# Optimization experiments

Hardware: AMD Instinct MI355X
Metric: run time of the kernel (lower is better)

Reference implementation:

```python
import jax, jax.numpy as jnp
import numpy as np

NUM_EMBEDDINGS = 1024
EMBEDDING_DIM = 256
COMMITMENT_COST = 0.25


def setup_inputs() -> dict:
    key = jax.random.key(0)
    k_z, k_e = jax.random.split(key)
    z = jax.random.normal(k_z, (8, EMBEDDING_DIM, 16, 16, 16), dtype=jnp.float32)
    # nn.Embedding weight initialized uniform(-1/K, 1/K)
    codebook = jax.random.uniform(
        k_e, (NUM_EMBEDDINGS, EMBEDDING_DIM), dtype=jnp.float32,
        minval=-1.0 / NUM_EMBEDDINGS, maxval=1.0 / NUM_EMBEDDINGS)
    return {"z": z, "codebook": codebook}


def reference(z, codebook):
    B, D, H, W, L = z.shape
    # (B, D, H, W, L) -> (B, H, W, L, D) -> (N, D)
    z_perm = jnp.transpose(z, (0, 2, 3, 4, 1))          # (B,H,W,L,D)
    z_flat = z_perm.reshape(-1, D)                       # (N,D)
    # squared-distance via expansion: ||z||^2 + ||e||^2 - 2 z.e^T
    distances = ((z_flat ** 2).sum(axis=1, keepdims=True)
                 + (codebook ** 2).sum(axis=1)
                 - 2.0 * z_flat @ codebook.T)            # (N,K)
    indices = jnp.argmin(distances, axis=1)              # (N,)
    quantized = codebook[indices].reshape(B, H, W, L, D)
    idx_out = indices.reshape(B, H, W, L)
    # losses (stop_gradient mirrors .detach())
    e_latent_loss = jnp.mean((jax.lax.stop_gradient(quantized) - z_perm) ** 2)
    q_latent_loss = jnp.mean((quantized - jax.lax.stop_gradient(z_perm)) ** 2)
    vq_loss = q_latent_loss + COMMITMENT_COST * e_latent_loss
    # straight-through estimator
    quant_st = z_perm + jax.lax.stop_gradient(quantized - z_perm)
    quant_out = jnp.transpose(quant_st, (0, 4, 1, 2, 3))  # (B,D,H,W,L)
    return quant_out, idx_out, vq_loss
```

## Files before the change

### kernel.cpp

```cpp
#include <hip/hip_runtime.h>
#include <hip/hip_bf16.h>


#define K_CODES 1024
#define DIM 256
#define N_TOK 32768
#define SPATIAL 4096
#define TOK_BLK 64
#define CAP 28
#define MARGIN 1e-3f

typedef __attribute__((ext_vector_type(8))) short short8;
typedef __attribute__((ext_vector_type(4))) float float4v;

#define WS_LOSS 0
#define WS_E2 16
#define WS_EB 2048

#define O_IDX (8 * DIM * SPATIAL)
#define O_LOSS (O_IDX + N_TOK)

__device__ __forceinline__ float np_pairwise128(const float* x) {
  float r[8];
#pragma unroll
  for (int j = 0; j < 8; j++) r[j] = x[j];
  for (int i = 8; i < 128; i += 8) {
#pragma unroll
    for (int j = 0; j < 8; j++) r[j] = __fadd_rn(r[j], x[i + j]);
  }
  return __fadd_rn(__fadd_rn(__fadd_rn(r[0], r[1]), __fadd_rn(r[2], r[3])),
                   __fadd_rn(__fadd_rn(r[4], r[5]), __fadd_rn(r[6], r[7])));
}

__device__ __forceinline__ short f2bf(float v) {
  unsigned u = __float_as_uint(v);
  u = (u + 0x7fffu + ((u >> 16) & 1u)) >> 16;
  return (short)u;
}

__global__ __launch_bounds__(256) void prep_kernel(const float* __restrict__ e,
                                                   float* __restrict__ ws) {
  __shared__ float sq[DIM];
  int k = blockIdx.x, d = threadIdx.x;
  float v = e[k * DIM + d];
  int stage = k >> 6, ct = (k >> 4) & 3, nn = k & 15;
  int f = d >> 5, q = (d >> 3) & 3, j = d & 7;
  int off = ((((stage * 4 + ct) * 8 + f) * 64 + (q * 16 + nn)) * 8 + j);
  ((short*)(ws + WS_EB))[off] = f2bf(v);
  sq[d] = __fmul_rn(v, v);
  __syncthreads();
  if (d == 0) {
    ws[WS_E2 + k] = __fadd_rn(np_pairwise128(sq), np_pairwise128(sq + 128));
    if (k == 0) ws[WS_LOSS] = 0.f;
  }
}

__global__ __launch_bounds__(256, 2) void main_kernel(const float* __restrict__ z,
                                                      const float* __restrict__ e,
                                                      float* __restrict__ ws,
                                                      float* __restrict__ out) {
  __shared__ __align__(16) short Bst[64 * 256];
  __shared__ unsigned short cand[TOK_BLK][CAP];
  __shared__ float cands[TOK_BLK][CAP];
  __shared__ float aminv[TOK_BLK];
  __shared__ int cnt[TOK_BLK];
  __shared__ float Szs[TOK_BLK];
  __shared__ int mini_sh[TOK_BLK];
  __shared__ float red[4];

  int tid = threadIdx.x, w = tid >> 6, lane = tid & 63;
  int quad = lane >> 4, nn = lane & 15;
  int n0 = blockIdx.x * TOK_BLK;
  int b = n0 >> 12, s0 = n0 & 4095;
  const float* zb = z + (size_t)b * DIM * SPATIAL + s0;
  const float* Se = ws + WS_E2;
  if (tid < TOK_BLK) cnt[tid] = 0;

  if (quad == 0) {
    const float* zp = zb + w * 16 + nn;
    float total = 0.f;
#pragma unroll
    for (int blk = 0; blk < 2; blk++) {
      float r[8];
#pragma unroll
      for (int j = 0; j < 8; j++) {
        float v = zp[(size_t)(blk * 128 + j) * SPATIAL];
        r[j] = __fmul_rn(v, v);
      }
      for (int i = 8; i < 128; i += 8) {
#pragma unroll
        for (int j = 0; j < 8; j++) {
          float v = zp[(size_t)(blk * 128 + i + j) * SPATIAL];
          r[j] = __fadd_rn(r[j], __fmul_rn(v, v));
        }
      }
      float res = __fadd_rn(__fadd_rn(__fadd_rn(r[0], r[1]), __fadd_rn(r[2], r[3])),
                            __fadd_rn(__fadd_rn(r[4], r[5]), __fadd_rn(r[6], r[7])));
      total = (blk == 0) ? res : __fadd_rn(total, res);
    }
    Szs[w * 16 + nn] = total;
  }

  int tokA = w * 16 + nn;
  short8 A[8];
#pragma unroll
  for (int f = 0; f < 8; f++) {
    short8 a;
#pragma unroll
    for (int j = 0; j < 8; j++) {
      int d = f * 32 + quad * 8 + j;
      a[j] = f2bf(zb[(size_t)d * SPATIAL + tokA]);
    }
    A[f] = a;
  }

  const uint4* eBg = (const uint4*)(ws + WS_EB);
  float thr[4] = {3.4e38f, 3.4e38f, 3.4e38f, 3.4e38f};
  for (int stage = 0; stage < 16; stage++) {
    __syncthreads();
#pragma unroll
    for (int i = 0; i < 8; i++)
      ((uint4*)Bst)[i * 256 + tid] = eBg[(size_t)stage * 2048 + i * 256 + tid];
    __syncthreads();

    for (int ct = 0; ct < 4; ct++) {
      int kbase = stage * 64 + ct * 16;
      float4v C = {0.f, 0.f, 0.f, 0.f};
      const short8* Bp = (const short8*)Bst + ct * 8 * 64;
#pragma unroll
      for (int f = 0; f < 8; f++) {
        short8 Bf = Bp[f * 64 + lane];
        C = __builtin_amdgcn_mfma_f32_16x16x32_bf16(A[f], Bf, C, 0, 0, 0);
      }
      float SeK = Se[kbase + nn];
      float sv[4];
      bool pr[4];
#pragma unroll
      for (int r = 0; r < 4; r++) {
        float s = fmaf(-2.f, C[r], SeK);
        float m = s;
        m = fminf(m, __shfl_xor(m, 1, 16));
        m = fminf(m, __shfl_xor(m, 2, 16));
        m = fminf(m, __shfl_xor(m, 4, 16));
        m = fminf(m, __shfl_xor(m, 8, 16));
        thr[r] = fminf(thr[r], m);
        sv[r] = s;
        pr[r] = s < thr[r] + MARGIN;
      }
      if (__ballot(pr[0] | pr[1] | pr[2] | pr[3])) {
#pragma unroll
        for (int r = 0; r < 4; r++) {
          unsigned long long bl = __ballot(pr[r]);
          unsigned grp = (unsigned)((bl >> (quad * 16)) & 0xffffULL);
          if (grp) {
            int tb = w * 16 + quad * 4 + r;
            int base = cnt[tb];
            if (pr[r]) {
              int pos = base + __popc(grp & ((1u << nn) - 1u));
              if (pos < CAP) {
                cand[tb][pos] = (unsigned short)(kbase + nn);
                cands[tb][pos] = sv[r];
              }
            }
            if (nn == 0) cnt[tb] = base + __popc(grp);
          }
        }
      }
    }
  }
#pragma unroll
  for (int r = 0; r < 4; r++)
    if (nn == 0) aminv[w * 16 + quad * 4 + r] = thr[r];

  int tb = w * 16 + nn;
  int cc = cnt[tb];
  int cl = cc < CAP ? cc : CAP;
  float bestD = 3.4e38f;
  int bestk = 0x7fffffff;
  {
    const float* zp = zb + tb;
    float amin = aminv[tb], Szn = Szs[tb];
    for (int c = quad; c < cl; c += 4) {
      if (cands[tb][c] >= amin + MARGIN) continue;
      int k = cand[tb][c];
      const float* er = e + (size_t)k * DIM;
      float acc = 0.f;
      for (int d = 0; d < DIM; d++) acc = fmaf(zp[(size_t)d * SPATIAL], er[d], acc);
      float D = __fsub_rn(__fadd_rn(Szn, Se[k]), __fmul_rn(2.f, acc));
      if (D < bestD || (D == bestD && k < bestk)) { bestD = D; bestk = k; }
    }
  }
#pragma unroll
  for (int off = 32; off >= 16; off >>= 1) {
    float oD = __shfl_down(bestD, off);
    int ok = __shfl_down(bestk, off);
    if (oD < bestD || (oD == bestD && ok < bestk)) { bestD = oD; bestk = ok; }
  }
  if (lane < 16 && cnt[w * 16 + lane] <= CAP) {
    mini_sh[w * 16 + lane] = bestk;
    out[O_IDX + n0 + w * 16 + lane] = (float)bestk;
  }
  for (int t = 0; t < 16; t++) {
    int tb2 = w * 16 + t;
    if (cnt[tb2] > CAP) {
      const float* zq = zb + tb2;
      float Szn = Szs[tb2];
      float bD = 3.4e38f;
      int bk = 0x7fffffff;
      for (int k = lane; k < K_CODES; k += 64) {
        const float* er = e + (size_t)k * DIM;
        float acc = 0.f;
        for (int d = 0; d < DIM; d++) acc = fmaf(zq[(size_t)d * SPATIAL], er[d], acc);
        float D = __fsub_rn(__fadd_rn(Szn, Se[k]), __fmul_rn(2.f, acc));
        if (D < bD || (D == bD && k < bk)) { bD = D; bk = k; }
      }
#pragma unroll
      for (int m = 1; m < 64; m <<= 1) {
        float oD = __shfl_xor(bD, m);
        int ok = __shfl_xor(bk, m);
        if (oD < bD || (oD == bD && ok < bk)) { bD = oD; bk = ok; }
      }
      if (lane == 0) {
        mini_sh[tb2] = bk;
        out[O_IDX + n0 + tb2] = (float)bk;
      }
    }
  }
  __syncthreads();

  int mten = mini_sh[lane];
  const float* erow = e + (size_t)mten * DIM;
  float* op = out + (size_t)b * DIM * SPATIAL + s0;
  float sumsq = 0.f;
  for (int i = 0; i < 64; i++) {
    int d = w * 64 + i;
    float v = erow[d];
    float zv = zb[(size_t)d * SPATIAL + lane];
    float df = __fsub_rn(v, zv);
    sumsq = fmaf(df, df, sumsq);
    op[(size_t)d * SPATIAL + lane] = v;
  }
#pragma unroll
  for (int o = 32; o > 0; o >>= 1) sumsq += __shfl_down(sumsq, o, 64);
  if (lane == 0) red[w] = sumsq;
  __syncthreads();
  if (tid == 0) atomicAdd(ws + WS_LOSS, red[0] + red[1] + red[2] + red[3]);
}

__global__ void loss_kernel(const float* __restrict__ ws, float* __restrict__ out) {
  out[O_LOSS] = 1.25f * ws[WS_LOSS] / 8388608.f;
}

extern "C" void kernel_launch(void* const* d_in, const int* in_sizes, int n_in,
                              void* d_out, int out_size, void* d_ws, size_t ws_size,
                              hipStream_t stream) {
  const float* z = (const float*)d_in[0];
  const float* e = (const float*)d_in[1];
  float* ws = (float*)d_ws;
  float* out = (float*)d_out;

  prep_kernel<<<K_CODES, 256, 0, stream>>>(e, ws);
  main_kernel<<<N_TOK / TOK_BLK, 256, 0, stream>>>(z, e, ws, out);
  loss_kernel<<<1, 1, 0, stream>>>(ws, out);
}
```

Baseline: 206.7 us.

## Double-buffer codebook stages via async LDS loads, parallelize norms, fuse loss kernel

Codebook bf16 tiles are now loaded straight into LDS with global_load_lds into two buffers, and the next-but-one stage is issued after each compute stage, so loads overlap the MFMA work. The z-norm computation is spread across all four quads with shuffle reduction instead of one quad, and prep writes 16-byte chunks. The separate loss kernel is removed; the last block, found with an atomic counter, writes the final loss. Unroll pragmas are added to the exact-rescore loops. The LDS footprint doubles, which may limit occupancy, and the hand-written waitcnt logic adds risk.

```diff
diff --git a/kernel.cpp b/kernel.cpp
--- a/kernel.cpp
+++ b/kernel.cpp
@@ -1,5 +1,4 @@
 #include <hip/hip_runtime.h>
-#include <hip/hip_bf16.h>
 
 
 #define K_CODES 1024
@@ -7,6 +6,7 @@
 #define N_TOK 32768
 #define SPATIAL 4096
 #define TOK_BLK 64
+#define NBLK (N_TOK / TOK_BLK)
 #define CAP 28
 #define MARGIN 1e-3f
 
@@ -14,23 +14,12 @@
 typedef __attribute__((ext_vector_type(4))) float float4v;
 
 #define WS_LOSS 0
+#define WS_CNT 8
 #define WS_E2 16
 #define WS_EB 2048
 
 #define O_IDX (8 * DIM * SPATIAL)
 #define O_LOSS (O_IDX + N_TOK)
-
-__device__ __forceinline__ float np_pairwise128(const float* x) {
-  float r[8];
-#pragma unroll
-  for (int j = 0; j < 8; j++) r[j] = x[j];
-  for (int i = 8; i < 128; i += 8) {
-#pragma unroll
-    for (int j = 0; j < 8; j++) r[j] = __fadd_rn(r[j], x[i + j]);
-  }
-  return __fadd_rn(__fadd_rn(__fadd_rn(r[0], r[1]), __fadd_rn(r[2], r[3])),
-                   __fadd_rn(__fadd_rn(r[4], r[5]), __fadd_rn(r[6], r[7])));
-}
 
 __device__ __forceinline__ short f2bf(float v) {
   unsigned u = __float_as_uint(v);
@@ -38,20 +27,58 @@
   return (short)u;
 }
 
+__device__ __forceinline__ void gload_lds16(const void* g, void* l) {
+  __builtin_amdgcn_global_load_lds(
+      (__attribute__((address_space(1))) unsigned*)g,
+      (__attribute__((address_space(3))) unsigned*)l, 16, 0, 0);
+}
+
+__device__ __forceinline__ void stage_issue(const uint4* eBg, short* lbuf,
+                                            int stage, int tid) {
+#pragma unroll
+  for (int i = 0; i < 8; i++)
+    gload_lds16(eBg + (size_t)stage * 2048 + i * 256 + tid,
+                lbuf + ((i * 256 + tid) << 3));
+}
+
 __global__ __launch_bounds__(256) void prep_kernel(const float* __restrict__ e,
                                                    float* __restrict__ ws) {
   __shared__ float sq[DIM];
+  __shared__ __align__(16) short sbf[DIM];
+  __shared__ float chv[16];
   int k = blockIdx.x, d = threadIdx.x;
   float v = e[k * DIM + d];
-  int stage = k >> 6, ct = (k >> 4) & 3, nn = k & 15;
-  int f = d >> 5, q = (d >> 3) & 3, j = d & 7;
-  int off = ((((stage * 4 + ct) * 8 + f) * 64 + (q * 16 + nn)) * 8 + j);
-  ((short*)(ws + WS_EB))[off] = f2bf(v);
+  sbf[d] = f2bf(v);
   sq[d] = __fmul_rn(v, v);
   __syncthreads();
+  if (d < 32) {
+    int f = d >> 2, q = d & 3;
+    int stage = k >> 6, ct = (k >> 4) & 3, nn = k & 15;
+    short8 chunk = *(const short8*)(sbf + f * 32 + q * 8);
+    int off8 = ((stage * 4 + ct) * 8 + f) * 64 + q * 16 + nn;
+    ((short8*)(ws + WS_EB))[off8] = chunk;
+  }
+  if (d < 16) {
+    int blkb = d >> 3, j = d & 7;
+    const float* x = sq + blkb * 128;
+    float c = x[j];
+#pragma unroll
+    for (int i = 1; i < 16; i++) c = __fadd_rn(c, x[i * 8 + j]);
+    chv[d] = c;
+  }
+  __syncthreads();
   if (d == 0) {
-    ws[WS_E2 + k] = __fadd_rn(np_pairwise128(sq), np_pairwise128(sq + 128));
-    if (k == 0) ws[WS_LOSS] = 0.f;
+    float a0 = __fadd_rn(__fadd_rn(chv[0], chv[1]), __fadd_rn(chv[2], chv[3]));
+    float a1 = __fadd_rn(__fadd_rn(chv[4], chv[5]), __fadd_rn(chv[6], chv[7]));
+    float resA = __fadd_rn(a0, a1);
+    float b0 = __fadd_rn(__fadd_rn(chv[8], chv[9]), __fadd_rn(chv[10], chv[11]));
+    float b1 = __fadd_rn(__fadd_rn(chv[12], chv[13]), __fadd_rn(chv[14], chv[15]));
+    float resB = __fadd_rn(b0, b1);
+    ws[WS_E2 + k] = __fadd_rn(resA, resB);
+    if (k == 0) {
+      ws[WS_LOSS] = 0.f;
+      ((unsigned*)ws)[WS_CNT] = 0u;
+    }
   }
 }
 
@@ -59,7 +86,7 @@
                                                       const float* __restrict__ e,
                                                       float* __restrict__ ws,
                                                       float* __restrict__ out) {
-  __shared__ __align__(16) short Bst[64 * 256];
+  __shared__ __align__(16) short Bst[2][64 * 256];
   __shared__ unsigned short cand[TOK_BLK][CAP];
   __shared__ float cands[TOK_BLK][CAP];
   __shared__ float aminv[TOK_BLK];
@@ -74,31 +101,32 @@
   int b = n0 >> 12, s0 = n0 & 4095;
   const float* zb = z + (size_t)b * DIM * SPATIAL + s0;
   const float* Se = ws + WS_E2;
+  const uint4* eBg = (const uint4*)(ws + WS_EB);
   if (tid < TOK_BLK) cnt[tid] = 0;
 
-  if (quad == 0) {
+  stage_issue(eBg, Bst[0], 0, tid);
+  stage_issue(eBg, Bst[1], 1, tid);
+  __builtin_amdgcn_sched_barrier(0);
+
+  {
     const float* zp = zb + w * 16 + nn;
-    float total = 0.f;
-#pragma unroll
-    for (int blk = 0; blk < 2; blk++) {
-      float r[8];
-#pragma unroll
-      for (int j = 0; j < 8; j++) {
-        float v = zp[(size_t)(blk * 128 + j) * SPATIAL];
-        r[j] = __fmul_rn(v, v);
-      }
-      for (int i = 8; i < 128; i += 8) {
-#pragma unroll
-        for (int j = 0; j < 8; j++) {
-          float v = zp[(size_t)(blk * 128 + i + j) * SPATIAL];
-          r[j] = __fadd_rn(r[j], __fmul_rn(v, v));
-        }
-      }
-      float res = __fadd_rn(__fadd_rn(__fadd_rn(r[0], r[1]), __fadd_rn(r[2], r[3])),
-                            __fadd_rn(__fadd_rn(r[4], r[5]), __fadd_rn(r[6], r[7])));
-      total = (blk == 0) ? res : __fadd_rn(total, res);
-    }
-    Szs[w * 16 + nn] = total;
+    float r[4];
+#pragma unroll
+    for (int t = 0; t < 4; t++) {
+      int c = quad * 4 + t, blkb = c >> 3, j = c & 7;
+      float v0 = zp[(size_t)(blkb * 128 + j) * SPATIAL];
+      r[t] = __fmul_rn(v0, v0);
+      for (int i = 1; i < 16; i++) {
+        float vv = zp[(size_t)(blkb * 128 + i * 8 + j) * SPATIAL];
+        r[t] = __fadd_rn(r[t], __fmul_rn(vv, vv));
+      }
+    }
+    float half = __fadd_rn(__fadd_rn(r[0], r[1]), __fadd_rn(r[2], r[3]));
+    float other = __shfl_xor(half, 16);
+    float resb = __fadd_rn(half, other);
+    float res_o = __shfl_xor(resb, 32);
+    float total = __fadd_rn(resb, res_o);
+    if (quad == 0) Szs[w * 16 + nn] = total;
   }
 
   int tokA = w * 16 + nn;
@@ -114,19 +142,23 @@
     A[f] = a;
   }
 
-  const uint4* eBg = (const uint4*)(ws + WS_EB);
+  __syncthreads();
+
   float thr[4] = {3.4e38f, 3.4e38f, 3.4e38f, 3.4e38f};
   for (int stage = 0; stage < 16; stage++) {
-    __syncthreads();
-#pragma unroll
-    for (int i = 0; i < 8; i++)
-      ((uint4*)Bst)[i * 256 + tid] = eBg[(size_t)stage * 2048 + i * 256 + tid];
-    __syncthreads();
+    if (stage == 15) {
+      asm volatile("s_waitcnt vmcnt(0)" ::: "memory");
+    } else {
+      asm volatile("s_waitcnt vmcnt(8)" ::: "memory");
+    }
+    __builtin_amdgcn_sched_barrier(0);
+    __builtin_amdgcn_s_barrier();
+    const short* Bbuf = Bst[stage & 1];
 
     for (int ct = 0; ct < 4; ct++) {
       int kbase = stage * 64 + ct * 16;
       float4v C = {0.f, 0.f, 0.f, 0.f};
-      const short8* Bp = (const short8*)Bst + ct * 8 * 64;
+      const short8* Bp = (const short8*)Bbuf + ct * 8 * 64;
 #pragma unroll
       for (int f = 0; f < 8; f++) {
         short8 Bf = Bp[f * 64 + lane];
@@ -167,6 +199,10 @@
         }
       }
     }
+
+    __builtin_amdgcn_s_barrier();
+    if (stage < 14) stage_issue(eBg, Bst[stage & 1], stage + 2, tid);
+    __builtin_amdgcn_sched_barrier(0);
   }
 #pragma unroll
   for (int r = 0; r < 4; r++)
@@ -185,6 +221,7 @@
       int k = cand[tb][c];
       const float* er = e + (size_t)k * DIM;
       float acc = 0.f;
+#pragma unroll 8
       for (int d = 0; d < DIM; d++) acc = fmaf(zp[(size_t)d * SPATIAL], er[d], acc);
       float D = __fsub_rn(__fadd_rn(Szn, Se[k]), __fmul_rn(2.f, acc));
       if (D < bestD || (D == bestD && k < bestk)) { bestD = D; bestk = k; }
@@ -210,6 +247,7 @@
       for (int k = lane; k < K_CODES; k += 64) {
         const float* er = e + (size_t)k * DIM;
         float acc = 0.f;
+#pragma unroll 8
         for (int d = 0; d < DIM; d++) acc = fmaf(zq[(size_t)d * SPATIAL], er[d], acc);
         float D = __fsub_rn(__fadd_rn(Szn, Se[k]), __fmul_rn(2.f, acc));
         if (D < bD || (D == bD && k < bk)) { bD = D; bk = k; }
@@ -244,11 +282,15 @@
   for (int o = 32; o > 0; o >>= 1) sumsq += __shfl_down(sumsq, o, 64);
   if (lane == 0) red[w] = sumsq;
   __syncthreads();
-  if (tid == 0) atomicAdd(ws + WS_LOSS, red[0] + red[1] + red[2] + red[3]);
-}
-
-__global__ void loss_kernel(const float* __restrict__ ws, float* __restrict__ out) {
-  out[O_LOSS] = 1.25f * ws[WS_LOSS] / 8388608.f;
+  if (tid == 0) {
+    atomicAdd(ws + WS_LOSS, red[0] + red[1] + red[2] + red[3]);
+    __threadfence();
+    unsigned t = atomicAdd((unsigned*)ws + WS_CNT, 1u);
+    if (t == NBLK - 1) {
+      float total = atomicAdd(ws + WS_LOSS, 0.f);
+      out[O_LOSS] = 1.25f * total / 8388608.f;
+    }
+  }
 }
 
 extern "C" void kernel_launch(void* const* d_in, const int* in_sizes, int n_in,
@@ -260,6 +302,5 @@
   float* out = (float*)d_out;
 
   prep_kernel<<<K_CODES, 256, 0, stream>>>(e, ws);
-  main_kernel<<<N_TOK / TOK_BLK, 256, 0, stream>>>(z, e, ws, out);
-  loss_kernel<<<1, 1, 0, stream>>>(ws, out);
-}
+  main_kernel<<<NBLK, 256, 0, stream>>>(z, e, ws, out);
+}
```

Result: slower. 219.2 us (+6.0%).
